# Kernel optimization log

Measured on AMD Instinct MI355X. Metric: run time of the kernel, lower is better.

## Reference

```python
import jax, jax.numpy as jnp
import numpy as np

HID = 2048   # hidden_size
H = 16       # num_attention_heads
KV = 2       # num_key_value_heads
HD = 256     # head_dim
S = 2048     # seq_len (prefill)
MAX_SEQ = 4096
EPS = 1e-6
RD = HD // 4          # partial RoPE dims (head_dim * 0.25)
SCALE = HD ** (-0.5)
GROUPS = H // KV


def setup_inputs() -> dict:
    key = jax.random.key(0)
    ks = jax.random.split(key, 10)
    hidden_in = jax.random.normal(ks[0], (1, S, HID), jnp.float32)
    ang = jax.random.uniform(ks[1], (1, S, RD), jnp.float32) * (2.0 * np.pi)
    cos = jnp.cos(ang)
    sin = jnp.sin(ang)
    w = 0.02
    q_proj_w = jax.random.normal(ks[2], (2 * H * HD, HID), jnp.float32) * w
    k_proj_w = jax.random.normal(ks[3], (KV * HD, HID), jnp.float32) * w
    v_proj_w = jax.random.normal(ks[4], (KV * HD, HID), jnp.float32) * w
    o_proj_w = jax.random.normal(ks[5], (HID, H * HD), jnp.float32) * w
    q_norm_w = jax.random.normal(ks[6], (HD,), jnp.float32) * 0.1
    k_norm_w = jax.random.normal(ks[7], (HD,), jnp.float32) * 0.1
    return dict(hidden_in=hidden_in, cos=cos, sin=sin,
                q_proj_w=q_proj_w, k_proj_w=k_proj_w, v_proj_w=v_proj_w,
                o_proj_w=o_proj_w, q_norm_w=q_norm_w, k_norm_w=k_norm_w)


def _rmsnorm(x, w):
    var = jnp.mean(x * x, axis=-1, keepdims=True)
    return x * jax.lax.rsqrt(var + EPS) * (1.0 + w)


def _rotate_half(x):
    x1, x2 = jnp.split(x, 2, axis=-1)
    return jnp.concatenate([-x2, x1], axis=-1)


def reference(hidden_in, cos, sin, q_proj_w, k_proj_w, v_proj_w, o_proj_w, q_norm_w, k_norm_w):
    # projections (F.linear => x @ W^T)
    qg = hidden_in @ q_proj_w.T                      # [1, S, 2*H*HD]
    k = hidden_in @ k_proj_w.T                       # [1, S, KV*HD]
    v = hidden_in @ v_proj_w.T

    qg = qg.reshape(1, S, H, 2 * HD)
    q, gate = qg[..., :HD], qg[..., HD:]             # chunk(2, dim=-1)
    gate = gate.reshape(1, S, H * HD)

    q = _rmsnorm(q, q_norm_w).transpose(0, 2, 1, 3)  # [1, H, S, HD]
    k = _rmsnorm(k.reshape(1, S, KV, HD), k_norm_w).transpose(0, 2, 1, 3)  # [1, KV, S, HD]
    v = v.reshape(1, S, KV, HD).transpose(0, 2, 1, 3)                      # [1, KV, S, HD]

    # partial RoPE on first RD dims
    c = cos[:, None, :, :]                           # [1, 1, S, RD]
    s = sin[:, None, :, :]
    q_rot, q_pass = q[..., :RD], q[..., RD:]
    k_rot, k_pass = k[..., :RD], k[..., RD:]
    q = jnp.concatenate([q_rot * c + _rotate_half(q_rot) * s, q_pass], axis=-1)
    k = jnp.concatenate([k_rot * c + _rotate_half(k_rot) * s, k_pass], axis=-1)

    # KV cache padded to max_seq
    zpad = jnp.zeros((1, KV, MAX_SEQ - S, HD), k.dtype)
    k_cache_out = jnp.concatenate([k, zpad], axis=2)
    v_cache_out = jnp.concatenate([v, zpad], axis=2)

    # GQA repeat
    k_r = jnp.repeat(k, GROUPS, axis=1)              # [1, H, S, HD]
    v_r = jnp.repeat(v, GROUPS, axis=1)

    causal = jnp.triu(jnp.full((S, S), -10000.0, jnp.float32), k=1)
    scores = jnp.einsum('bhqd,bhkd->bhqk', q, k_r) * SCALE + causal
    attn_w = jax.nn.softmax(scores, axis=-1)
    attn = jnp.einsum('bhqk,bhkd->bhqd', attn_w, v_r)
    attn = attn.transpose(0, 2, 1, 3).reshape(1, S, H * HD)

    attn = attn * jax.nn.sigmoid(gate)
    hidden_out = attn @ o_proj_w.T                   # [1, S, HID]
    return hidden_out, k_cache_out, v_cache_out
```

## Files before the change

### kernel.cpp

```cpp
#include <hip/hip_runtime.h>

#define S_LEN 2048
#define HID 2048
#define NH 16
#define NKV 2
#define HD 256
#define MAXSEQ 4096
#define NALL 9216
#define RD 64

typedef __attribute__((ext_vector_type(8))) short short8_t;
typedef __attribute__((ext_vector_type(4))) float float4_t;

#define DPPF(x, ctrl) __builtin_bit_cast(float, __builtin_amdgcn_update_dpp( \
    __builtin_bit_cast(int, x), __builtin_bit_cast(int, x), ctrl, 0xF, 0xF, false))

__device__ __forceinline__ unsigned short f2b(float f) {
  union { float f; unsigned u; } v; v.f = f;
  unsigned u = v.u;
  return (unsigned short)((u + 0x7FFFu + ((u >> 16) & 1u)) >> 16);
}

__device__ __forceinline__ void gload_lds16(const void* g, void* l) {
  __builtin_amdgcn_global_load_lds(
      (const __attribute__((address_space(1))) void*)g,
      (__attribute__((address_space(3))) void*)l, 16, 0, 0);
}

__global__ void cvt_bf16(const float* __restrict__ src, unsigned short* __restrict__ dst, int n4) {
  int i = blockIdx.x * blockDim.x + threadIdx.x;
  if (i < n4) {
    float4 v = ((const float4*)src)[i];
    short4 o;
    o.x = (short)f2b(v.x); o.y = (short)f2b(v.y);
    o.z = (short)f2b(v.z); o.w = (short)f2b(v.w);
    ((short4*)dst)[i] = o;
  }
}

template<int BM, int BN, int MI, int NI>
__global__ __launch_bounds__(256, 2) void gemm_bt(
    const unsigned short* __restrict__ A, const unsigned short* __restrict__ B,
    float* __restrict__ C, int M, int N, int K) {
  constexpr int BK = 64;
  __shared__ unsigned short As[BM * BK];
  __shared__ unsigned short Bs[BN * BK];
  const int tid = threadIdx.x;
  const int lane = tid & 63;
  const int w = tid >> 6;
  const int wr = w >> 1, wc = w & 1;
  const int l15 = lane & 15, l4 = lane >> 4;
  const int M0 = blockIdx.y * BM, N0 = blockIdx.x * BN;
  float4_t acc[MI][NI] = {};
  for (int kt = 0; kt < K; kt += BK) {
    __syncthreads();
#pragma unroll
    for (int i = 0; i < BM/32; ++i) {
      int c = tid + i*256;
      int row = c >> 3;
      gload_lds16(A + (size_t)(M0 + row)*K + kt + ((c & 7) ^ (row & 7))*8, (char*)As + c*16);
    }
#pragma unroll
    for (int i = 0; i < BN/32; ++i) {
      int c = tid + i*256;
      int row = c >> 3;
      gload_lds16(B + (size_t)(N0 + row)*K + kt + ((c & 7) ^ (row & 7))*8, (char*)Bs + c*16);
    }
    __syncthreads();
#pragma unroll
    for (int ks = 0; ks < 2; ++ks) {
      short8_t af[MI], bf[NI];
#pragma unroll
      for (int mi = 0; mi < MI; ++mi) {
        int row = wr*(BM/2) + mi*16 + l15;
        af[mi] = *(const short8_t*)&As[row*BK + ((ks*4 + l4) ^ (l15 & 7))*8];
      }
#pragma unroll
      for (int ni = 0; ni < NI; ++ni) {
        int row = wc*(BN/2) + ni*16 + l15;
        bf[ni] = *(const short8_t*)&Bs[row*BK + ((ks*4 + l4) ^ (l15 & 7))*8];
      }
#pragma unroll
      for (int mi = 0; mi < MI; ++mi)
#pragma unroll
        for (int ni = 0; ni < NI; ++ni)
          acc[mi][ni] = __builtin_amdgcn_mfma_f32_16x16x32_bf16(af[mi], bf[ni], acc[mi][ni], 0, 0, 0);
    }
  }
#pragma unroll
  for (int mi = 0; mi < MI; ++mi) {
    int rb = M0 + wr*(BM/2) + mi*16 + l4*4;
#pragma unroll
    for (int ni = 0; ni < NI; ++ni) {
      int col = N0 + wc*(BN/2) + ni*16 + l15;
#pragma unroll
      for (int r = 0; r < 4; ++r)
        C[(size_t)(rb + r)*N + col] = acc[mi][ni][r];
    }
  }
}

__global__ void postproc(const float* __restrict__ C1,
                         const float* __restrict__ cosb, const float* __restrict__ sinb,
                         const float* __restrict__ qnw, const float* __restrict__ knw,
                         unsigned short* __restrict__ qb, unsigned short* __restrict__ kb,
                         unsigned short* __restrict__ vtb,
                         float* __restrict__ kcache, float* __restrict__ vcache) {
  const int w = threadIdx.x >> 6, lane = threadIdx.x & 63;
  const int s = blockIdx.x*4 + w;
  const int t = blockIdx.y;
  const int d = lane*4;
  const float* rowp;
  if (t < 16)      rowp = C1 + (size_t)s*NALL + t*512;
  else if (t < 18) rowp = C1 + (size_t)s*NALL + 8192 + (t-16)*256;
  else             rowp = C1 + (size_t)s*NALL + 8704 + (t-18)*256;
  float4 x = *(const float4*)(rowp + d);
  if (t >= 18) {
    int kvi = t - 18;
    *(float4*)(vcache + (size_t)kvi*MAXSEQ*HD + (size_t)s*HD + d) = x;
    unsigned short* vt = vtb + (size_t)kvi*HD*S_LEN;
    vt[(size_t)(d+0)*S_LEN + s] = f2b(x.x);
    vt[(size_t)(d+1)*S_LEN + s] = f2b(x.y);
    vt[(size_t)(d+2)*S_LEN + s] = f2b(x.z);
    vt[(size_t)(d+3)*S_LEN + s] = f2b(x.w);
    return;
  }
  float ss = x.x*x.x + x.y*x.y + x.z*x.z + x.w*x.w;
#pragma unroll
  for (int o = 32; o >= 1; o >>= 1) ss += __shfl_xor(ss, o, 64);
  float rn = rsqrtf(ss*(1.0f/256.0f) + 1e-6f);
  const float* nw = (t < 16) ? qnw : knw;
  float4 g = *(const float4*)(nw + d);
  float4 y;
  y.x = x.x*rn*(1.f+g.x); y.y = x.y*rn*(1.f+g.y);
  y.z = x.z*rn*(1.f+g.z); y.w = x.w*rn*(1.f+g.w);
  float px = __shfl_xor(y.x, 8, 64);
  float py = __shfl_xor(y.y, 8, 64);
  float pz = __shfl_xor(y.z, 8, 64);
  float pw = __shfl_xor(y.w, 8, 64);
  if (lane < 16) {
    float sgn = (lane & 8) ? 1.f : -1.f;
    float4 cs = *(const float4*)(cosb + (size_t)s*RD + d);
    float4 sn = *(const float4*)(sinb + (size_t)s*RD + d);
    y.x = y.x*cs.x + sgn*px*sn.x;
    y.y = y.y*cs.y + sgn*py*sn.y;
    y.z = y.z*cs.z + sgn*pz*sn.z;
    y.w = y.w*cs.w + sgn*pw*sn.w;
  }
  if (t < 16) {
    const float qs = 0.0625f * 1.44269504088896f;
    short4 o;
    o.x = (short)f2b(y.x*qs); o.y = (short)f2b(y.y*qs);
    o.z = (short)f2b(y.z*qs); o.w = (short)f2b(y.w*qs);
    *(short4*)(qb + (size_t)t*S_LEN*HD + (size_t)s*HD + d) = o;
  } else {
    int kvi = t - 16;
    *(float4*)(kcache + (size_t)kvi*MAXSEQ*HD + (size_t)s*HD + d) = y;
    short4 o;
    o.x = (short)f2b(y.x); o.y = (short)f2b(y.y);
    o.z = (short)f2b(y.z); o.w = (short)f2b(y.w);
    *(short4*)(kb + (size_t)kvi*S_LEN*HD + (size_t)s*HD + d) = o;
  }
}

__global__ __launch_bounds__(256, 2) void attn_kernel(
    const unsigned short* __restrict__ qb, const unsigned short* __restrict__ kb,
    const unsigned short* __restrict__ vtb, const float* __restrict__ C1,
    unsigned short* __restrict__ attnb) {
  __shared__ char smem[73728];
  unsigned short* Ks  = (unsigned short*)smem;
  unsigned short* VTs = (unsigned short*)(smem + 32768);
  const int tid = threadIdx.x, lane = tid & 63, w = tid >> 6;
  const int l15 = lane & 15, l4 = lane >> 4;
  const int b = blockIdx.x;
  const int i2 = b >> 1;
  const int h = i2 & 15;
  const int t16 = i2 >> 4;
  const int qt = (b & 1) ? (31 - t16) : t16;
  const int kv = h >> 3;
  const int q0 = qt * 64;
  const unsigned short* Qb = qb + (size_t)h*S_LEN*HD;
  const unsigned short* Kb = kb + (size_t)kv*S_LEN*HD;
  const unsigned short* Vb = vtb + (size_t)kv*HD*S_LEN;
  unsigned short* Pw = (unsigned short*)(smem + 65536 + w*2048);
  const int qrow = q0 + w*16 + l15;
  short8_t qf[8];
#pragma unroll
  for (int kk = 0; kk < 8; ++kk)
    qf[kk] = *(const short8_t*)(Qb + (size_t)qrow*HD + kk*32 + l4*8);
  float4_t oacc[16] = {};
  float m_run[4] = {-1e30f, -1e30f, -1e30f, -1e30f};
  float l_run[4] = {0.f, 0.f, 0.f, 0.f};
  for (int kbI = 0; kbI <= qt; ++kbI) {
    const int k0 = kbI * 64;
    __syncthreads();
#pragma unroll
    for (int i = 0; i < 8; ++i) {
      int c = tid + i*256;
      int row = c >> 5;
      gload_lds16(Kb + (size_t)(k0 + row)*HD + ((c & 31) ^ (row & 7))*8, (char*)Ks + c*16);
    }
#pragma unroll
    for (int i = 0; i < 8; ++i) {
      int c = tid + i*256;
      int row = c >> 3;
      gload_lds16(Vb + (size_t)row*S_LEN + k0 + ((c & 7) ^ (row & 7))*8, (char*)VTs + c*16);
    }
    __syncthreads();
    float4_t sacc[4] = {};
#pragma unroll
    for (int nt = 0; nt < 4; ++nt)
#pragma unroll
      for (int kk = 0; kk < 8; ++kk) {
        short8_t bfr = *(const short8_t*)&Ks[(nt*16 + l15)*HD + (((kk*4 + l4) ^ (l15 & 7)))*8];
        sacc[nt] = __builtin_amdgcn_mfma_f32_16x16x32_bf16(qf[kk], bfr, sacc[nt], 0, 0, 0);
      }
    if (kbI == qt) {
#pragma unroll
      for (int nt = 0; nt < 4; ++nt)
#pragma unroll
        for (int r = 0; r < 4; ++r)
          if (nt*16 + l15 > w*16 + l4*4 + r) sacc[nt][r] = -1e30f;
    }
    float alpha[4], p[4][4];
#pragma unroll
    for (int r = 0; r < 4; ++r) {
      float m0 = fmaxf(fmaxf(sacc[0][r], sacc[1][r]), fmaxf(sacc[2][r], sacc[3][r]));
      m0 = fmaxf(m0, DPPF(m0, 0xB1));
      m0 = fmaxf(m0, DPPF(m0, 0x4E));
      m0 = fmaxf(m0, DPPF(m0, 0x141));
      m0 = fmaxf(m0, DPPF(m0, 0x140));
      float mnew = fmaxf(m_run[r], m0);
      alpha[r] = exp2f(m_run[r] - mnew);
      m_run[r] = mnew;
      float sum = 0.f;
#pragma unroll
      for (int nt = 0; nt < 4; ++nt) {
        p[nt][r] = exp2f(sacc[nt][r] - mnew);
        sum += p[nt][r];
      }
      sum += DPPF(sum, 0xB1);
      sum += DPPF(sum, 0x4E);
      sum += DPPF(sum, 0x141);
      sum += DPPF(sum, 0x140);
      l_run[r] = l_run[r]*alpha[r] + sum;
    }
#pragma unroll
    for (int nt2 = 0; nt2 < 16; ++nt2) {
      oacc[nt2][0] *= alpha[0];
      oacc[nt2][1] *= alpha[1];
      oacc[nt2][2] *= alpha[2];
      oacc[nt2][3] *= alpha[3];
    }
#pragma unroll
    for (int nt = 0; nt < 4; ++nt)
#pragma unroll
      for (int r = 0; r < 4; ++r) {
        int prow = l4*4 + r;
        int pcol = nt*16 + l15;
        Pw[prow*64 + (((pcol >> 3) ^ (prow & 7)))*8 + (pcol & 7)] = f2b(p[nt][r]);
      }
    short8_t pf0 = *(const short8_t*)&Pw[l15*64 + ((l4 ^ (l15 & 7)))*8];
    short8_t pf1 = *(const short8_t*)&Pw[l15*64 + (((l4 ^ 4) ^ (l15 & 7)))*8];
#pragma unroll
    for (int nt2 = 0; nt2 < 16; ++nt2) {
      int vrow = nt2*16 + l15;
      short8_t v0 = *(const short8_t*)&VTs[vrow*64 + ((l4 ^ (l15 & 7)))*8];
      short8_t v1 = *(const short8_t*)&VTs[vrow*64 + (((l4 ^ 4) ^ (l15 & 7)))*8];
      oacc[nt2] = __builtin_amdgcn_mfma_f32_16x16x32_bf16(pf0, v0, oacc[nt2], 0, 0, 0);
      oacc[nt2] = __builtin_amdgcn_mfma_f32_16x16x32_bf16(pf1, v1, oacc[nt2], 0, 0, 0);
    }
  }
  float inv_l[4];
#pragma unroll
  for (int r = 0; r < 4; ++r) inv_l[r] = 1.f / l_run[r];
  const int srow0 = q0 + w*16 + l4*4;
#pragma unroll
  for (int nt2 = 0; nt2 < 16; ++nt2) {
    int dim = nt2*16 + l15;
#pragma unroll
    for (int r = 0; r < 4; ++r) {
      int srow = srow0 + r;
      float gv = C1[(size_t)srow*NALL + h*512 + 256 + dim];
      float sg = 1.f / (1.f + __expf(-gv));
      attnb[(size_t)srow*(NH*HD) + h*HD + dim] = f2b(oacc[nt2][r] * inv_l[r] * sg);
    }
  }
}

extern "C" void kernel_launch(void* const* d_in, const int* in_sizes, int n_in,
                              void* d_out, int out_size, void* d_ws, size_t ws_size,
                              hipStream_t stream) {
  const float* hidden = (const float*)d_in[0];
  const float* cosb   = (const float*)d_in[1];
  const float* sinb   = (const float*)d_in[2];
  const float* qw     = (const float*)d_in[3];
  const float* kw     = (const float*)d_in[4];
  const float* vw     = (const float*)d_in[5];
  const float* ow     = (const float*)d_in[6];
  const float* qnw    = (const float*)d_in[7];
  const float* knw    = (const float*)d_in[8];
  float* out    = (float*)d_out;
  float* kcache = out + (size_t)S_LEN*HID;
  float* vcache = kcache + (size_t)NKV*MAXSEQ*HD;

  char* ws = (char*)d_ws;
  size_t off = 0;
  auto alloc = [&](size_t bytes) -> char* {
    char* p = ws + off; off += (bytes + 255) & ~(size_t)255; return p;
  };
  unsigned short* hidb  = (unsigned short*)alloc((size_t)S_LEN*HID*2);
  unsigned short* wallb = (unsigned short*)alloc((size_t)NALL*HID*2);
  unsigned short* wob   = (unsigned short*)alloc((size_t)HID*NH*HD*2);
  float*          C1    = (float*)alloc((size_t)S_LEN*NALL*4);
  unsigned short* qb    = (unsigned short*)alloc((size_t)NH*S_LEN*HD*2);
  unsigned short* kb    = (unsigned short*)alloc((size_t)NKV*S_LEN*HD*2);
  unsigned short* vtb   = (unsigned short*)alloc((size_t)NKV*HD*S_LEN*2);
  unsigned short* attnb = (unsigned short*)alloc((size_t)S_LEN*NH*HD*2);

  cvt_bf16<<<(S_LEN*HID/4 + 255)/256, 256, 0, stream>>>(hidden, hidb, S_LEN*HID/4);
  cvt_bf16<<<(8192*HID/4 + 255)/256, 256, 0, stream>>>(qw, wallb, 8192*HID/4);
  cvt_bf16<<<(512*HID/4 + 255)/256, 256, 0, stream>>>(kw, wallb + (size_t)8192*HID, 512*HID/4);
  cvt_bf16<<<(512*HID/4 + 255)/256, 256, 0, stream>>>(vw, wallb + (size_t)8704*HID, 512*HID/4);
  cvt_bf16<<<(HID*NH*HD/4 + 255)/256, 256, 0, stream>>>(ow, wob, HID*NH*HD/4);

  for (int kvi = 0; kvi < NKV; ++kvi) {
    hipMemsetAsync(kcache + (size_t)kvi*MAXSEQ*HD + (size_t)S_LEN*HD, 0,
                   (size_t)(MAXSEQ - S_LEN)*HD*4, stream);
    hipMemsetAsync(vcache + (size_t)kvi*MAXSEQ*HD + (size_t)S_LEN*HD, 0,
                   (size_t)(MAXSEQ - S_LEN)*HD*4, stream);
  }

  gemm_bt<128,128,4,4><<<dim3(NALL/128, S_LEN/128), 256, 0, stream>>>(
      hidb, wallb, C1, S_LEN, NALL, HID);

  postproc<<<dim3(S_LEN/4, 20), 256, 0, stream>>>(
      C1, cosb, sinb, qnw, knw, qb, kb, vtb, kcache, vcache);

  attn_kernel<<<512, 256, 0, stream>>>(qb, kb, vtb, C1, attnb);

  gemm_bt<128,128,4,4><<<dim3(HID/128, S_LEN/128), 256, 0, stream>>>(
      attnb, wob, out, S_LEN, HID, NH*HD);
}
```

Baseline: 477.8 us.

## Register-block attention over two query groups per wave and fuse conversion kernels

Attention blocks shrink to two waves, each processing 32 query rows so every K fragment read from LDS feeds two MFMAs, and the query-tile ordering is remapped for load balance. The five bf16 conversion launches and four cache memsets are merged into one kernel to cut launch overhead. The trade is fewer resident waves per CU and higher register pressure, which may reduce latency hiding.

New measurement: 637.5 us. +33.4%, slower.

```diff
diff --git a/kernel.cpp b/kernel.cpp
--- a/kernel.cpp
+++ b/kernel.cpp
@@ -27,14 +27,35 @@
       (__attribute__((address_space(3))) void*)l, 16, 0, 0);
 }
 
-__global__ void cvt_bf16(const float* __restrict__ src, unsigned short* __restrict__ dst, int n4) {
-  int i = blockIdx.x * blockDim.x + threadIdx.x;
-  if (i < n4) {
-    float4 v = ((const float4*)src)[i];
+__global__ void fused_cvt(const float* __restrict__ hidden, const float* __restrict__ qw,
+                          const float* __restrict__ kw, const float* __restrict__ vw,
+                          const float* __restrict__ ow,
+                          unsigned short* __restrict__ hidb, unsigned short* __restrict__ wallb,
+                          unsigned short* __restrict__ wob,
+                          float* __restrict__ kcache, float* __restrict__ vcache) {
+  const long i = (long)blockIdx.x * 256 + threadIdx.x;
+  const long N0 = 1048576, N1 = N0 + 4194304, N2 = N1 + 262144, N3 = N2 + 262144,
+             N4 = N3 + 2097152;
+  if (i < N4) {
+    const float* s; unsigned short* d; long j;
+    if (i < N0)      { s = hidden; d = hidb;  j = i; }
+    else if (i < N1) { s = qw; d = wallb;                        j = i - N0; }
+    else if (i < N2) { s = kw; d = wallb + (size_t)8192*HID;     j = i - N1; }
+    else if (i < N3) { s = vw; d = wallb + (size_t)8704*HID;     j = i - N2; }
+    else             { s = ow; d = wob;                          j = i - N3; }
+    float4 v = ((const float4*)s)[j];
     short4 o;
     o.x = (short)f2b(v.x); o.y = (short)f2b(v.y);
     o.z = (short)f2b(v.z); o.w = (short)f2b(v.w);
-    ((short4*)dst)[i] = o;
+    ((short4*)d)[j] = o;
+  } else {
+    long j = i - N4;
+    int region = (int)(j >> 17);
+    long o = j & 131071;
+    float* base = (region < 2 ? kcache : vcache)
+                + (size_t)(region & 1) * MAXSEQ * HD + (size_t)S_LEN * HD;
+    float4 z; z.x = 0.f; z.y = 0.f; z.z = 0.f; z.w = 0.f;
+    ((float4*)base)[o] = z;
   }
 }
 
@@ -163,7 +184,7 @@
   }
 }
 
-__global__ __launch_bounds__(256, 2) void attn_kernel(
+__global__ __launch_bounds__(128, 1) void attn_kernel(
     const unsigned short* __restrict__ qb, const unsigned short* __restrict__ kb,
     const unsigned short* __restrict__ vtb, const float* __restrict__ C1,
     unsigned short* __restrict__ attnb) {
@@ -176,114 +197,134 @@
   const int i2 = b >> 1;
   const int h = i2 & 15;
   const int t16 = i2 >> 4;
-  const int qt = (b & 1) ? (31 - t16) : t16;
+  const int gt = (t16 < 8) ? t16 : 23 - t16;
+  const int qt = (b & 1) ? (31 - gt) : gt;
   const int kv = h >> 3;
   const int q0 = qt * 64;
   const unsigned short* Qb = qb + (size_t)h*S_LEN*HD;
   const unsigned short* Kb = kb + (size_t)kv*S_LEN*HD;
   const unsigned short* Vb = vtb + (size_t)kv*HD*S_LEN;
-  unsigned short* Pw = (unsigned short*)(smem + 65536 + w*2048);
-  const int qrow = q0 + w*16 + l15;
-  short8_t qf[8];
-#pragma unroll
-  for (int kk = 0; kk < 8; ++kk)
-    qf[kk] = *(const short8_t*)(Qb + (size_t)qrow*HD + kk*32 + l4*8);
-  float4_t oacc[16] = {};
-  float m_run[4] = {-1e30f, -1e30f, -1e30f, -1e30f};
-  float l_run[4] = {0.f, 0.f, 0.f, 0.f};
+  unsigned short* Pw = (unsigned short*)(smem + 65536 + w*4096);
+  short8_t qf[2][8];
+#pragma unroll
+  for (int g = 0; g < 2; ++g)
+#pragma unroll
+    for (int kk = 0; kk < 8; ++kk)
+      qf[g][kk] = *(const short8_t*)(Qb + (size_t)(q0 + w*32 + g*16 + l15)*HD + kk*32 + l4*8);
+  float4_t oacc[2][16] = {};
+  float m_run[2][4], l_run[2][4];
+#pragma unroll
+  for (int g = 0; g < 2; ++g)
+#pragma unroll
+    for (int r = 0; r < 4; ++r) { m_run[g][r] = -1e30f; l_run[g][r] = 0.f; }
   for (int kbI = 0; kbI <= qt; ++kbI) {
     const int k0 = kbI * 64;
     __syncthreads();
 #pragma unroll
-    for (int i = 0; i < 8; ++i) {
-      int c = tid + i*256;
+    for (int i = 0; i < 16; ++i) {
+      int c = tid + i*128;
       int row = c >> 5;
       gload_lds16(Kb + (size_t)(k0 + row)*HD + ((c & 31) ^ (row & 7))*8, (char*)Ks + c*16);
     }
 #pragma unroll
-    for (int i = 0; i < 8; ++i) {
-      int c = tid + i*256;
+    for (int i = 0; i < 16; ++i) {
+      int c = tid + i*128;
       int row = c >> 3;
       gload_lds16(Vb + (size_t)row*S_LEN + k0 + ((c & 7) ^ (row & 7))*8, (char*)VTs + c*16);
     }
     __syncthreads();
-    float4_t sacc[4] = {};
+    float4_t sacc[2][4] = {};
 #pragma unroll
     for (int nt = 0; nt < 4; ++nt)
 #pragma unroll
       for (int kk = 0; kk < 8; ++kk) {
-        short8_t bfr = *(const short8_t*)&Ks[(nt*16 + l15)*HD + (((kk*4 + l4) ^ (l15 & 7)))*8];
-        sacc[nt] = __builtin_amdgcn_mfma_f32_16x16x32_bf16(qf[kk], bfr, sacc[nt], 0, 0, 0);
+        short8_t bfr = *(const short8_t*)&Ks[(nt*16 + l15)*HD + ((kk*4 + l4) ^ (l15 & 7))*8];
+        sacc[0][nt] = __builtin_amdgcn_mfma_f32_16x16x32_bf16(qf[0][kk], bfr, sacc[0][nt], 0, 0, 0);
+        sacc[1][nt] = __builtin_amdgcn_mfma_f32_16x16x32_bf16(qf[1][kk], bfr, sacc[1][nt], 0, 0, 0);
       }
     if (kbI == qt) {
 #pragma unroll
+      for (int g = 0; g < 2; ++g)
+#pragma unroll
+        for (int nt = 0; nt < 4; ++nt)
+#pragma unroll
+          for (int r = 0; r < 4; ++r)
+            if (nt*16 + l15 > w*32 + g*16 + l4*4 + r) sacc[g][nt][r] = -1e30f;
+    }
+#pragma unroll
+    for (int g = 0; g < 2; ++g) {
+      float alpha[4], p[4][4];
+#pragma unroll
+      for (int r = 0; r < 4; ++r) {
+        float m0 = fmaxf(fmaxf(sacc[g][0][r], sacc[g][1][r]), fmaxf(sacc[g][2][r], sacc[g][3][r]));
+        m0 = fmaxf(m0, DPPF(m0, 0xB1));
+        m0 = fmaxf(m0, DPPF(m0, 0x4E));
+        m0 = fmaxf(m0, DPPF(m0, 0x141));
+        m0 = fmaxf(m0, DPPF(m0, 0x140));
+        float mnew = fmaxf(m_run[g][r], m0);
+        alpha[r] = exp2f(m_run[g][r] - mnew);
+        m_run[g][r] = mnew;
+        float sum = 0.f;
+#pragma unroll
+        for (int nt = 0; nt < 4; ++nt) {
+          p[nt][r] = exp2f(sacc[g][nt][r] - mnew);
+          sum += p[nt][r];
+        }
+        sum += DPPF(sum, 0xB1);
+        sum += DPPF(sum, 0x4E);
+        sum += DPPF(sum, 0x141);
+        sum += DPPF(sum, 0x140);
+        l_run[g][r] = l_run[g][r]*alpha[r] + sum;
+      }
+#pragma unroll
+      for (int nt2 = 0; nt2 < 16; ++nt2) {
+        oacc[g][nt2][0] *= alpha[0];
+        oacc[g][nt2][1] *= alpha[1];
+        oacc[g][nt2][2] *= alpha[2];
+        oacc[g][nt2][3] *= alpha[3];
+      }
+#pragma unroll
       for (int nt = 0; nt < 4; ++nt)
 #pragma unroll
-        for (int r = 0; r < 4; ++r)
-          if (nt*16 + l15 > w*16 + l4*4 + r) sacc[nt][r] = -1e30f;
-    }
-    float alpha[4], p[4][4];
-#pragma unroll
-    for (int r = 0; r < 4; ++r) {
-      float m0 = fmaxf(fmaxf(sacc[0][r], sacc[1][r]), fmaxf(sacc[2][r], sacc[3][r]));
-      m0 = fmaxf(m0, DPPF(m0, 0xB1));
-      m0 = fmaxf(m0, DPPF(m0, 0x4E));
-      m0 = fmaxf(m0, DPPF(m0, 0x141));
-      m0 = fmaxf(m0, DPPF(m0, 0x140));
-      float mnew = fmaxf(m_run[r], m0);
-      alpha[r] = exp2f(m_run[r] - mnew);
-      m_run[r] = mnew;
-      float sum = 0.f;
-#pragma unroll
-      for (int nt = 0; nt < 4; ++nt) {
-        p[nt][r] = exp2f(sacc[nt][r] - mnew);
-        sum += p[nt][r];
-      }
-      sum += DPPF(sum, 0xB1);
-      sum += DPPF(sum, 0x4E);
-      sum += DPPF(sum, 0x141);
-      sum += DPPF(sum, 0x140);
-      l_run[r] = l_run[r]*alpha[r] + sum;
-    }
-#pragma unroll
-    for (int nt2 = 0; nt2 < 16; ++nt2) {
-      oacc[nt2][0] *= alpha[0];
-      oacc[nt2][1] *= alpha[1];
-      oacc[nt2][2] *= alpha[2];
-      oacc[nt2][3] *= alpha[3];
-    }
-#pragma unroll
-    for (int nt = 0; nt < 4; ++nt)
-#pragma unroll
-      for (int r = 0; r < 4; ++r) {
-        int prow = l4*4 + r;
-        int pcol = nt*16 + l15;
-        Pw[prow*64 + (((pcol >> 3) ^ (prow & 7)))*8 + (pcol & 7)] = f2b(p[nt][r]);
-      }
-    short8_t pf0 = *(const short8_t*)&Pw[l15*64 + ((l4 ^ (l15 & 7)))*8];
-    short8_t pf1 = *(const short8_t*)&Pw[l15*64 + (((l4 ^ 4) ^ (l15 & 7)))*8];
+        for (int r = 0; r < 4; ++r) {
+          int prow = g*16 + l4*4 + r;
+          int pcol = nt*16 + l15;
+          Pw[prow*64 + (((pcol >> 3) ^ (prow & 7)))*8 + (pcol & 7)] = f2b(p[nt][r]);
+        }
+    }
+    short8_t pf[2][2];
+#pragma unroll
+    for (int g = 0; g < 2; ++g) {
+      pf[g][0] = *(const short8_t*)&Pw[(g*16 + l15)*64 + ((l4 ^ (l15 & 7)))*8];
+      pf[g][1] = *(const short8_t*)&Pw[(g*16 + l15)*64 + (((l4 ^ 4) ^ (l15 & 7)))*8];
+    }
 #pragma unroll
     for (int nt2 = 0; nt2 < 16; ++nt2) {
       int vrow = nt2*16 + l15;
       short8_t v0 = *(const short8_t*)&VTs[vrow*64 + ((l4 ^ (l15 & 7)))*8];
       short8_t v1 = *(const short8_t*)&VTs[vrow*64 + (((l4 ^ 4) ^ (l15 & 7)))*8];
-      oacc[nt2] = __builtin_amdgcn_mfma_f32_16x16x32_bf16(pf0, v0, oacc[nt2], 0, 0, 0);
-      oacc[nt2] = __builtin_amdgcn_mfma_f32_16x16x32_bf16(pf1, v1, oacc[nt2], 0, 0, 0);
-    }
-  }
-  float inv_l[4];
-#pragma unroll
-  for (int r = 0; r < 4; ++r) inv_l[r] = 1.f / l_run[r];
-  const int srow0 = q0 + w*16 + l4*4;
-#pragma unroll
-  for (int nt2 = 0; nt2 < 16; ++nt2) {
-    int dim = nt2*16 + l15;
-#pragma unroll
-    for (int r = 0; r < 4; ++r) {
-      int srow = srow0 + r;
-      float gv = C1[(size_t)srow*NALL + h*512 + 256 + dim];
-      float sg = 1.f / (1.f + __expf(-gv));
-      attnb[(size_t)srow*(NH*HD) + h*HD + dim] = f2b(oacc[nt2][r] * inv_l[r] * sg);
+      oacc[0][nt2] = __builtin_amdgcn_mfma_f32_16x16x32_bf16(pf[0][0], v0, oacc[0][nt2], 0, 0, 0);
+      oacc[0][nt2] = __builtin_amdgcn_mfma_f32_16x16x32_bf16(pf[0][1], v1, oacc[0][nt2], 0, 0, 0);
+      oacc[1][nt2] = __builtin_amdgcn_mfma_f32_16x16x32_bf16(pf[1][0], v0, oacc[1][nt2], 0, 0, 0);
+      oacc[1][nt2] = __builtin_amdgcn_mfma_f32_16x16x32_bf16(pf[1][1], v1, oacc[1][nt2], 0, 0, 0);
+    }
+  }
+#pragma unroll
+  for (int g = 0; g < 2; ++g) {
+    float inv_l[4];
+#pragma unroll
+    for (int r = 0; r < 4; ++r) inv_l[r] = 1.f / l_run[g][r];
+    const int srow0 = q0 + w*32 + g*16 + l4*4;
+#pragma unroll
+    for (int nt2 = 0; nt2 < 16; ++nt2) {
+      int dim = nt2*16 + l15;
+#pragma unroll
+      for (int r = 0; r < 4; ++r) {
+        int srow = srow0 + r;
+        float gv = C1[(size_t)srow*NALL + h*512 + 256 + dim];
+        float sg = 1.f / (1.f + __expf(-gv));
+        attnb[(size_t)srow*(NH*HD) + h*HD + dim] = f2b(oacc[g][nt2][r] * inv_l[r] * sg);
+      }
     }
   }
 }
@@ -318,18 +359,8 @@
   unsigned short* vtb   = (unsigned short*)alloc((size_t)NKV*HD*S_LEN*2);
   unsigned short* attnb = (unsigned short*)alloc((size_t)S_LEN*NH*HD*2);
 
-  cvt_bf16<<<(S_LEN*HID/4 + 255)/256, 256, 0, stream>>>(hidden, hidb, S_LEN*HID/4);
-  cvt_bf16<<<(8192*HID/4 + 255)/256, 256, 0, stream>>>(qw, wallb, 8192*HID/4);
-  cvt_bf16<<<(512*HID/4 + 255)/256, 256, 0, stream>>>(kw, wallb + (size_t)8192*HID, 512*HID/4);
-  cvt_bf16<<<(512*HID/4 + 255)/256, 256, 0, stream>>>(vw, wallb + (size_t)8704*HID, 512*HID/4);
-  cvt_bf16<<<(HID*NH*HD/4 + 255)/256, 256, 0, stream>>>(ow, wob, HID*NH*HD/4);
-
-  for (int kvi = 0; kvi < NKV; ++kvi) {
-    hipMemsetAsync(kcache + (size_t)kvi*MAXSEQ*HD + (size_t)S_LEN*HD, 0,
-                   (size_t)(MAXSEQ - S_LEN)*HD*4, stream);
-    hipMemsetAsync(vcache + (size_t)kvi*MAXSEQ*HD + (size_t)S_LEN*HD, 0,
-                   (size_t)(MAXSEQ - S_LEN)*HD*4, stream);
-  }
+  fused_cvt<<<32768, 256, 0, stream>>>(hidden, qw, kw, vw, ow,
+                                       hidb, wallb, wob, kcache, vcache);
 
   gemm_bt<128,128,4,4><<<dim3(NALL/128, S_LEN/128), 256, 0, stream>>>(
       hidb, wallb, C1, S_LEN, NALL, HID);
@@ -337,7 +368,7 @@
   postproc<<<dim3(S_LEN/4, 20), 256, 0, stream>>>(
       C1, cosb, sinb, qnw, knw, qb, kb, vtb, kcache, vcache);
 
-  attn_kernel<<<512, 256, 0, stream>>>(qb, kb, vtb, C1, attnb);
+  attn_kernel<<<512, 128, 0, stream>>>(qb, kb, vtb, C1, attnb);
 
   gemm_bt<128,128,4,4><<<dim3(HID/128, S_LEN/128), 256, 0, stream>>>(
       attnb, wob, out, S_LEN, HID, NH*HD);
```

## Fuse conversion kernels with cache zeroing; halve attention key block size

Applied to the files above, without the earlier changes.

Replaces five bf16 conversion launches and four memsets with one fused kernel that converts the inputs and zero-fills the padded KV cache regions, removing launch overhead. The attention kernel now processes 32-key blocks instead of 64, with smaller LDS buffers and an adjusted swizzle, and applies the causal mask on the last two blocks. The smaller tiles cut LDS use, which may allow more resident blocks and wastes less work on the diagonal, at the cost of twice as many iterations and barriers.

Result: no change. 471.1 us (-1.4%).

```diff
diff --git a/kernel.cpp b/kernel.cpp
--- a/kernel.cpp
+++ b/kernel.cpp
@@ -27,14 +27,35 @@
       (__attribute__((address_space(3))) void*)l, 16, 0, 0);
 }
 
-__global__ void cvt_bf16(const float* __restrict__ src, unsigned short* __restrict__ dst, int n4) {
-  int i = blockIdx.x * blockDim.x + threadIdx.x;
-  if (i < n4) {
-    float4 v = ((const float4*)src)[i];
+__global__ void fused_cvt(const float* __restrict__ hidden, const float* __restrict__ qw,
+                          const float* __restrict__ kw, const float* __restrict__ vw,
+                          const float* __restrict__ ow,
+                          unsigned short* __restrict__ hidb, unsigned short* __restrict__ wallb,
+                          unsigned short* __restrict__ wob,
+                          float* __restrict__ kcache, float* __restrict__ vcache) {
+  const long i = (long)blockIdx.x * 256 + threadIdx.x;
+  const long N0 = 1048576, N1 = N0 + 4194304, N2 = N1 + 262144, N3 = N2 + 262144,
+             N4 = N3 + 2097152;
+  if (i < N4) {
+    const float* s; unsigned short* d; long j;
+    if (i < N0)      { s = hidden; d = hidb;  j = i; }
+    else if (i < N1) { s = qw; d = wallb;                        j = i - N0; }
+    else if (i < N2) { s = kw; d = wallb + (size_t)8192*HID;     j = i - N1; }
+    else if (i < N3) { s = vw; d = wallb + (size_t)8704*HID;     j = i - N2; }
+    else             { s = ow; d = wob;                          j = i - N3; }
+    float4 v = ((const float4*)s)[j];
     short4 o;
     o.x = (short)f2b(v.x); o.y = (short)f2b(v.y);
     o.z = (short)f2b(v.z); o.w = (short)f2b(v.w);
-    ((short4*)dst)[i] = o;
+    ((short4*)d)[j] = o;
+  } else {
+    long j = i - N4;
+    int region = (int)(j >> 17);
+    long o = j & 131071;
+    float* base = (region < 2 ? kcache : vcache)
+                + (size_t)(region & 1) * MAXSEQ * HD + (size_t)S_LEN * HD;
+    float4 z; z.x = 0.f; z.y = 0.f; z.z = 0.f; z.w = 0.f;
+    ((float4*)base)[o] = z;
   }
 }
 
@@ -167,9 +188,9 @@
     const unsigned short* __restrict__ qb, const unsigned short* __restrict__ kb,
     const unsigned short* __restrict__ vtb, const float* __restrict__ C1,
     unsigned short* __restrict__ attnb) {
-  __shared__ char smem[73728];
+  __shared__ char smem[36864];
   unsigned short* Ks  = (unsigned short*)smem;
-  unsigned short* VTs = (unsigned short*)(smem + 32768);
+  unsigned short* VTs = (unsigned short*)(smem + 16384);
   const int tid = threadIdx.x, lane = tid & 63, w = tid >> 6;
   const int l15 = lane & 15, l4 = lane >> 4;
   const int b = blockIdx.x;
@@ -182,7 +203,7 @@
   const unsigned short* Qb = qb + (size_t)h*S_LEN*HD;
   const unsigned short* Kb = kb + (size_t)kv*S_LEN*HD;
   const unsigned short* Vb = vtb + (size_t)kv*HD*S_LEN;
-  unsigned short* Pw = (unsigned short*)(smem + 65536 + w*2048);
+  unsigned short* Pw = (unsigned short*)(smem + 32768 + w*1024);
   const int qrow = q0 + w*16 + l15;
   short8_t qf[8];
 #pragma unroll
@@ -191,41 +212,42 @@
   float4_t oacc[16] = {};
   float m_run[4] = {-1e30f, -1e30f, -1e30f, -1e30f};
   float l_run[4] = {0.f, 0.f, 0.f, 0.f};
-  for (int kbI = 0; kbI <= qt; ++kbI) {
-    const int k0 = kbI * 64;
+  const int nIter = 2*qt + 2;
+  for (int kbI = 0; kbI < nIter; ++kbI) {
+    const int k0 = kbI * 32;
     __syncthreads();
 #pragma unroll
-    for (int i = 0; i < 8; ++i) {
+    for (int i = 0; i < 4; ++i) {
       int c = tid + i*256;
       int row = c >> 5;
       gload_lds16(Kb + (size_t)(k0 + row)*HD + ((c & 31) ^ (row & 7))*8, (char*)Ks + c*16);
     }
 #pragma unroll
-    for (int i = 0; i < 8; ++i) {
+    for (int i = 0; i < 4; ++i) {
       int c = tid + i*256;
-      int row = c >> 3;
-      gload_lds16(Vb + (size_t)row*S_LEN + k0 + ((c & 7) ^ (row & 7))*8, (char*)VTs + c*16);
+      int row = c >> 2;
+      gload_lds16(Vb + (size_t)row*S_LEN + k0 + ((c & 3) ^ ((row >> 1) & 3))*8, (char*)VTs + c*16);
     }
     __syncthreads();
-    float4_t sacc[4] = {};
-#pragma unroll
-    for (int nt = 0; nt < 4; ++nt)
+    float4_t sacc[2] = {};
+#pragma unroll
+    for (int nt = 0; nt < 2; ++nt)
 #pragma unroll
       for (int kk = 0; kk < 8; ++kk) {
-        short8_t bfr = *(const short8_t*)&Ks[(nt*16 + l15)*HD + (((kk*4 + l4) ^ (l15 & 7)))*8];
+        short8_t bfr = *(const short8_t*)&Ks[(nt*16 + l15)*HD + ((kk*4 + l4) ^ (l15 & 7))*8];
         sacc[nt] = __builtin_amdgcn_mfma_f32_16x16x32_bf16(qf[kk], bfr, sacc[nt], 0, 0, 0);
       }
-    if (kbI == qt) {
-#pragma unroll
-      for (int nt = 0; nt < 4; ++nt)
+    if (kbI >= 2*qt) {
+#pragma unroll
+      for (int nt = 0; nt < 2; ++nt)
 #pragma unroll
         for (int r = 0; r < 4; ++r)
-          if (nt*16 + l15 > w*16 + l4*4 + r) sacc[nt][r] = -1e30f;
-    }
-    float alpha[4], p[4][4];
+          if (k0 + nt*16 + l15 > q0 + w*16 + l4*4 + r) sacc[nt][r] = -1e30f;
+    }
+    float alpha[4], p[2][4];
 #pragma unroll
     for (int r = 0; r < 4; ++r) {
-      float m0 = fmaxf(fmaxf(sacc[0][r], sacc[1][r]), fmaxf(sacc[2][r], sacc[3][r]));
+      float m0 = fmaxf(sacc[0][r], sacc[1][r]);
       m0 = fmaxf(m0, DPPF(m0, 0xB1));
       m0 = fmaxf(m0, DPPF(m0, 0x4E));
       m0 = fmaxf(m0, DPPF(m0, 0x141));
@@ -235,7 +257,7 @@
       m_run[r] = mnew;
       float sum = 0.f;
 #pragma unroll
-      for (int nt = 0; nt < 4; ++nt) {
+      for (int nt = 0; nt < 2; ++nt) {
         p[nt][r] = exp2f(sacc[nt][r] - mnew);
         sum += p[nt][r];
       }
@@ -253,22 +275,19 @@
       oacc[nt2][3] *= alpha[3];
     }
 #pragma unroll
-    for (int nt = 0; nt < 4; ++nt)
+    for (int nt = 0; nt < 2; ++nt)
 #pragma unroll
       for (int r = 0; r < 4; ++r) {
         int prow = l4*4 + r;
         int pcol = nt*16 + l15;
-        Pw[prow*64 + (((pcol >> 3) ^ (prow & 7)))*8 + (pcol & 7)] = f2b(p[nt][r]);
-      }
-    short8_t pf0 = *(const short8_t*)&Pw[l15*64 + ((l4 ^ (l15 & 7)))*8];
-    short8_t pf1 = *(const short8_t*)&Pw[l15*64 + (((l4 ^ 4) ^ (l15 & 7)))*8];
+        Pw[prow*32 + (((pcol >> 3) ^ ((prow >> 1) & 3)))*8 + (pcol & 7)] = f2b(p[nt][r]);
+      }
+    short8_t pf = *(const short8_t*)&Pw[l15*32 + ((l4 ^ ((l15 >> 1) & 3)))*8];
 #pragma unroll
     for (int nt2 = 0; nt2 < 16; ++nt2) {
       int vrow = nt2*16 + l15;
-      short8_t v0 = *(const short8_t*)&VTs[vrow*64 + ((l4 ^ (l15 & 7)))*8];
-      short8_t v1 = *(const short8_t*)&VTs[vrow*64 + (((l4 ^ 4) ^ (l15 & 7)))*8];
-      oacc[nt2] = __builtin_amdgcn_mfma_f32_16x16x32_bf16(pf0, v0, oacc[nt2], 0, 0, 0);
-      oacc[nt2] = __builtin_amdgcn_mfma_f32_16x16x32_bf16(pf1, v1, oacc[nt2], 0, 0, 0);
+      short8_t v0 = *(const short8_t*)&VTs[vrow*32 + ((l4 ^ ((vrow >> 1) & 3)))*8];
+      oacc[nt2] = __builtin_amdgcn_mfma_f32_16x16x32_bf16(pf, v0, oacc[nt2], 0, 0, 0);
     }
   }
   float inv_l[4];
@@ -318,18 +337,8 @@
   unsigned short* vtb   = (unsigned short*)alloc((size_t)NKV*HD*S_LEN*2);
   unsigned short* attnb = (unsigned short*)alloc((size_t)S_LEN*NH*HD*2);
 
-  cvt_bf16<<<(S_LEN*HID/4 + 255)/256, 256, 0, stream>>>(hidden, hidb, S_LEN*HID/4);
-  cvt_bf16<<<(8192*HID/4 + 255)/256, 256, 0, stream>>>(qw, wallb, 8192*HID/4);
-  cvt_bf16<<<(512*HID/4 + 255)/256, 256, 0, stream>>>(kw, wallb + (size_t)8192*HID, 512*HID/4);
-  cvt_bf16<<<(512*HID/4 + 255)/256, 256, 0, stream>>>(vw, wallb + (size_t)8704*HID, 512*HID/4);
-  cvt_bf16<<<(HID*NH*HD/4 + 255)/256, 256, 0, stream>>>(ow, wob, HID*NH*HD/4);
-
-  for (int kvi = 0; kvi < NKV; ++kvi) {
-    hipMemsetAsync(kcache + (size_t)kvi*MAXSEQ*HD + (size_t)S_LEN*HD, 0,
-                   (size_t)(MAXSEQ - S_LEN)*HD*4, stream);
-    hipMemsetAsync(vcache + (size_t)kvi*MAXSEQ*HD + (size_t)S_LEN*HD, 0,
-                   (size_t)(MAXSEQ - S_LEN)*HD*4, stream);
-  }
+  fused_cvt<<<32768, 256, 0, stream>>>(hidden, qw, kw, vw, ow,
+                                       hidb, wallb, wob, kcache, vcache);
 
   gemm_bt<128,128,4,4><<<dim3(NALL/128, S_LEN/128), 256, 0, stream>>>(
       hidb, wallb, C1, S_LEN, NALL, HID);
```
